# Performance work log

Hardware: AMD Instinct MI355X
Metric: run time of the kernel (lower is better)

## Reference

```python
import jax, jax.numpy as jnp
import numpy as np
import math

N_HEAD = 16
N_KV_HEAD = 4
N_EMBD = 2048
HEAD_DIM = N_EMBD // N_HEAD  # 128
SCALE = 1.0 / math.sqrt(HEAD_DIM)
B, T = 2, 2048


def setup_inputs() -> dict:
    key = jax.random.key(0)
    ks = jax.random.split(key, 5)
    s = 0.02
    x = jax.random.normal(ks[0], (B, T, N_EMBD), dtype=jnp.float32)
    wq = jax.random.normal(ks[1], (N_EMBD, N_EMBD), dtype=jnp.float32) * s
    wk = jax.random.normal(ks[2], (N_KV_HEAD * HEAD_DIM, N_EMBD), dtype=jnp.float32) * s
    wv = jax.random.normal(ks[3], (N_KV_HEAD * HEAD_DIM, N_EMBD), dtype=jnp.float32) * s
    wo = jax.random.normal(ks[4], (N_EMBD, N_EMBD), dtype=jnp.float32) * s
    return {"x": x, "wq": wq, "wk": wk, "wv": wv, "wo": wo}


def _forward(x, wq, wk, wv, wo):
    b, t, _ = x.shape
    # Linear layers: y = x @ W.T  (torch Linear weight is (out,in))
    q = (x @ wq.T).reshape(b, t, N_HEAD, HEAD_DIM).transpose(0, 2, 1, 3)      # (B,H,T,D)
    k = (x @ wk.T).reshape(b, t, N_KV_HEAD, HEAD_DIM).transpose(0, 2, 1, 3)  # (B,Hkv,T,D)
    v = (x @ wv.T).reshape(b, t, N_KV_HEAD, HEAD_DIM).transpose(0, 2, 1, 3)
    groups = N_HEAD // N_KV_HEAD
    k = jnp.repeat(k, groups, axis=1)  # repeat_interleave over head dim -> (B,H,T,D)
    v = jnp.repeat(v, groups, axis=1)
    # Causal mask: True above diagonal (masked-out positions)
    mask = jnp.triu(jnp.ones((t, t), dtype=bool), k=1)[None, None]  # (1,1,T,T)
    scores = jnp.einsum('bhqd,bhkd->bhqk', q, k) * SCALE
    scores = jnp.where(mask, -jnp.inf, scores)
    attn = jax.nn.softmax(scores, axis=-1)
    attn = jnp.where(mask, 0.0, attn)
    y = jnp.einsum('bhqk,bhkd->bhqd', attn, v)       # (B,H,T,D)
    y = y.transpose(0, 2, 1, 3).reshape(b, t, N_EMBD)
    return y @ wo.T


def reference(x, wq, wk, wv, wo):
    return _forward(x, wq, wk, wv, wo)
```

## Files before the change

### kernel.cpp

```cpp
#include <hip/hip_runtime.h>
#include <cstdint>
#include <cstddef>

typedef __bf16 bf16_t;
typedef __bf16 bf16x8 __attribute__((ext_vector_type(8)));
typedef __bf16 bf16x4 __attribute__((ext_vector_type(4)));
typedef float f32x4 __attribute__((ext_vector_type(4)));

#define GL2LDS16(gptr, lptr)                                                   \
  __builtin_amdgcn_global_load_lds(                                            \
      (__attribute__((address_space(1))) void*)(gptr),                         \
      (__attribute__((address_space(3))) void*)(lptr), 16, 0, 0)

__device__ __forceinline__ float fast_exp2(float x) {
  float r;
  asm volatile("v_exp_f32 %0, %1" : "=v"(r) : "v"(x));
  return r;
}

#define BATCH 2
#define T_SEQ 2048
#define NH 16
#define NKV 4
#define HD 128
#define EMB 2048
#define KVDIM (NKV * HD)
#define MROWS (BATCH * T_SEQ)

__global__ void cvt_all(const float4* __restrict__ x,  const float4* __restrict__ wq,
                        const float4* __restrict__ wk, const float4* __restrict__ wv,
                        const float4* __restrict__ wo,
                        bf16x4* __restrict__ xb,  bf16x4* __restrict__ wqb,
                        bf16x4* __restrict__ wkb, bf16x4* __restrict__ wvb,
                        bf16x4* __restrict__ wob) {
  const int blk = blockIdx.x;
  const float4* src;
  bf16x4* dst;
  int base;
  if (blk < 8192)       { src = x;  dst = xb;  base = blk; }
  else if (blk < 12288) { src = wq; dst = wqb; base = blk - 8192; }
  else if (blk < 13312) { src = wk; dst = wkb; base = blk - 12288; }
  else if (blk < 14336) { src = wv; dst = wvb; base = blk - 13312; }
  else                  { src = wo; dst = wob; base = blk - 14336; }
  const int i = base * 256 + threadIdx.x;
  const float4 v = src[i];
  dst[i] = bf16x4{(__bf16)v.x, (__bf16)v.y, (__bf16)v.z, (__bf16)v.w};
}

#define BK8 64
#define NT8 (EMB / BK8)

__global__ __launch_bounds__(512, 2)
void gemm_qkv8(const bf16_t* __restrict__ A,
               const bf16_t* __restrict__ Wq, const bf16_t* __restrict__ Wk,
               const bf16_t* __restrict__ Wv,
               bf16_t* __restrict__ Qb, bf16_t* __restrict__ Kb,
               bf16_t* __restrict__ Vt, float qalpha)
{
  __shared__ bf16_t lds[2][512 * 64];

  const int tid  = threadIdx.x;
  const int lane = tid & 63;
  const int wv   = tid >> 6;
  const int l15  = lane & 15;
  const int lq   = lane >> 4;

  const int bid0 = blockIdx.x;
  const int bid  = (bid0 & 7) * 24 + (bid0 >> 3);
  const int mt = bid / 12, nt = bid % 12;
  const int m0 = mt * 256;

  const bf16_t* Bmat; int ncol0, seg;
  if (nt < 8)       { Bmat = Wq; ncol0 = nt * 256;        seg = 0; }
  else if (nt < 10) { Bmat = Wk; ncol0 = (nt - 8) * 256;  seg = 1; }
  else              { Bmat = Wv; ncol0 = (nt - 10) * 256; seg = 2; }

  const int wm = (wv >> 2) * 128;
  const int wn = (wv & 3) * 64;

  f32x4 acc[8][4] = {};

  auto stage = [&](int dbuf, int tsrc, int h) {
    const int k0 = tsrc * BK8;
    const bf16_t* src = (h < 2) ? A : Bmat;
    const int rbase = (h < 2) ? (m0 + h * 128) : (ncol0 + (h - 2) * 128);
    bf16_t* dst = &lds[dbuf][h * 8192];
#pragma unroll
    for (int r = 0; r < 2; ++r) {
      const int c = r * 512 + tid;
      const int row = c >> 3, p = c & 7;
      const int sb = p ^ (row & 7);
      GL2LDS16(src + (size_t)(rbase + row) * EMB + k0 + sb * 8, dst + c * 8);
    }
  };

  auto ldA = [&](int buf, int half, bf16x8 (&dst)[4][2]) {
#pragma unroll
    for (int i = 0; i < 4; ++i) {
      const int row = wm + half * 64 + i * 16 + l15;
#pragma unroll
      for (int ks = 0; ks < 2; ++ks)
        dst[i][ks] = *(const bf16x8*)&lds[buf][row * 64 + (((ks * 4 + lq) ^ (row & 7)) * 8)];
    }
  };
  auto ldB = [&](int buf, int half, bf16x8 (&dst)[2][2]) {
#pragma unroll
    for (int j = 0; j < 2; ++j) {
      const int row = 256 + wn + half * 32 + j * 16 + l15;
#pragma unroll
      for (int ks = 0; ks < 2; ++ks)
        dst[j][ks] = *(const bf16x8*)&lds[buf][row * 64 + (((ks * 4 + lq) ^ (row & 7)) * 8)];
    }
  };
  auto mm = [&](bf16x8 (&Af)[4][2], bf16x8 (&Bf)[2][2], int ai, int bj) {
    __builtin_amdgcn_s_setprio(1);
#pragma unroll
    for (int ks = 0; ks < 2; ++ks)
#pragma unroll
      for (int i = 0; i < 4; ++i)
#pragma unroll
        for (int j = 0; j < 2; ++j)
          acc[ai + i][bj + j] = __builtin_amdgcn_mfma_f32_16x16x32_bf16(
              Af[i][ks], Bf[j][ks], acc[ai + i][bj + j], 0, 0, 0);
    __builtin_amdgcn_s_setprio(0);
  };

  stage(0, 0, 0); stage(0, 0, 1); stage(0, 0, 2); stage(0, 0, 3);
  stage(1, 1, 2); stage(1, 1, 0); stage(1, 1, 3);
  asm volatile("s_waitcnt vmcnt(6)" ::: "memory");
  __builtin_amdgcn_s_barrier();

  bf16x8 al[4][2], ah[4][2], bX[2][2], bY[2][2];
  ldA(0, 0, al);
  ldB(0, 0, bX);

  auto body = [&](int cur, int t, bf16x8 (&b01)[2][2], bf16x8 (&b23)[2][2]) {
    const int nxt = cur ^ 1;
    const int tn1 = (t + 1 < NT8) ? t + 1 : NT8 - 1;
    const int tn2 = (t + 2 < NT8) ? t + 2 : NT8 - 1;

    stage(nxt, tn1, 1);
    ldB(cur, 1, b23);
    mm(al, b01, 0, 0);
    __builtin_amdgcn_s_barrier();

    ldA(cur, 1, ah);
    mm(al, b23, 0, 2);
    __builtin_amdgcn_s_barrier();

    stage(cur, tn2, 2);
    mm(ah, b23, 4, 2);
    __builtin_amdgcn_s_barrier();

    asm volatile("s_waitcnt vmcnt(2)" ::: "memory");
    stage(cur, tn2, 0);
    stage(cur, tn2, 3);
    ldA(nxt, 0, al);
    ldB(nxt, 0, b23);
    mm(ah, b01, 4, 0);
    __builtin_amdgcn_s_barrier();
  };

#pragma unroll 1
  for (int tt = 0; tt < NT8; tt += 2) {
    body(0, tt,     bX, bY);
    body(1, tt + 1, bY, bX);
  }
  asm volatile("s_waitcnt vmcnt(0)" ::: "memory");

  if (seg == 0) {
#pragma unroll
    for (int i = 0; i < 8; ++i) {
      const int rbase = m0 + wm + i * 16 + lq * 4;
#pragma unroll
      for (int j = 0; j < 4; ++j) {
        const int col = ncol0 + wn + j * 16 + l15;
#pragma unroll
        for (int r = 0; r < 4; ++r)
          Qb[(size_t)(rbase + r) * EMB + col] = (bf16_t)(acc[i][j][r] * qalpha);
      }
    }
  } else if (seg == 1) {
#pragma unroll
    for (int i = 0; i < 8; ++i) {
      const int rbase = m0 + wm + i * 16 + lq * 4;
#pragma unroll
      for (int j = 0; j < 4; ++j) {
        const int col = ncol0 + wn + j * 16 + l15;
#pragma unroll
        for (int r = 0; r < 4; ++r)
          Kb[(size_t)(rbase + r) * KVDIM + col] = (bf16_t)acc[i][j][r];
      }
    }
  } else {
    const int bb = m0 >> 11;
    const int mloc0 = (m0 & 2047) + wm + lq * 4;
#pragma unroll
    for (int i = 0; i < 8; ++i) {
      const int mloc = mloc0 + i * 16;
#pragma unroll
      for (int j = 0; j < 4; ++j) {
        const int d = ncol0 + wn + j * 16 + l15;
        *(bf16x4*)(Vt + (size_t)(bb * KVDIM + d) * T_SEQ + mloc) =
            bf16x4{(__bf16)acc[i][j][0], (__bf16)acc[i][j][1],
                   (__bf16)acc[i][j][2], (__bf16)acc[i][j][3]};
      }
    }
  }
}

__global__ __launch_bounds__(256, 2)
void gemm_out(const bf16_t* __restrict__ A, const bf16_t* __restrict__ Bm,
              float* __restrict__ C, int M, int N, int K)
{
  __shared__ bf16_t As[128 * 64];
  __shared__ bf16_t Bs[128 * 64];

  const int tid  = threadIdx.x;
  const int lane = tid & 63;
  const int wv   = tid >> 6;
  const int m0 = blockIdx.y * 128;
  const int n0 = blockIdx.x * 128;
  const int wm = (wv >> 1) * 64;
  const int wn = (wv & 1) * 64;
  const int l15 = lane & 15;
  const int lq  = lane >> 4;

  f32x4 acc[4][4] = {};
  const int srow = tid >> 3;
  const int scol = (tid & 7) * 8;

  for (int k0 = 0; k0 < K; k0 += 64) {
#pragma unroll
    for (int r = 0; r < 4; ++r) {
      const int row = r * 32 + srow;
      GL2LDS16(A + (size_t)(m0 + row) * K + k0 + scol, As + row * 64 + scol);
    }
#pragma unroll
    for (int r = 0; r < 4; ++r) {
      const int row = r * 32 + srow;
      GL2LDS16(Bm + (size_t)(n0 + row) * K + k0 + scol, Bs + row * 64 + scol);
    }
    __syncthreads();

#pragma unroll
    for (int ks = 0; ks < 2; ++ks) {
      const int kc = ks * 32 + lq * 8;
      bf16x8 af[4], bf[4];
#pragma unroll
      for (int i = 0; i < 4; ++i)
        af[i] = *(const bf16x8*)(As + (wm + i * 16 + l15) * 64 + kc);
#pragma unroll
      for (int j = 0; j < 4; ++j)
        bf[j] = *(const bf16x8*)(Bs + (wn + j * 16 + l15) * 64 + kc);
#pragma unroll
      for (int i = 0; i < 4; ++i)
#pragma unroll
        for (int j = 0; j < 4; ++j)
          acc[i][j] = __builtin_amdgcn_mfma_f32_16x16x32_bf16(af[i], bf[j], acc[i][j], 0, 0, 0);
    }
    __syncthreads();
  }

#pragma unroll
  for (int i = 0; i < 4; ++i) {
    const int rbase = m0 + wm + i * 16 + lq * 4;
#pragma unroll
    for (int j = 0; j < 4; ++j) {
      const int col = n0 + wn + j * 16 + l15;
#pragma unroll
      for (int r = 0; r < 4; ++r)
        C[(size_t)(rbase + r) * N + col] = acc[i][j][r];
    }
  }
}

#define PSTR 72

__global__ __launch_bounds__(256, 2)
void attn_fwd(const bf16_t* __restrict__ Q, const bf16_t* __restrict__ Kg,
              const bf16_t* __restrict__ Vt, bf16_t* __restrict__ Y)
{
  __shared__ bf16_t Ks[2][64 * 128];
  __shared__ bf16_t Vs[2][128 * 64];
  __shared__ bf16_t Ps[4][16 * PSTR];

  const int tid  = threadIdx.x;
  const int lane = tid & 63;
  const int wv   = tid >> 6;
  const int l15  = lane & 15;
  const int lq   = lane >> 4;
  const int h  = blockIdx.y;
  const int b  = blockIdx.z;
  const int hkv = h >> 2;
  bf16_t* Psw = Ps[wv];

  auto stage = [&](int kt, int bufsel) {
    const int base_t = b * T_SEQ + kt * 64;
#pragma unroll
    for (int r = 0; r < 4; ++r) {
      const int c = r * 256 + tid;
      const int row = c >> 4, p = c & 15;
      const int sb = p ^ (row & 7);
      GL2LDS16(Kg + (size_t)(base_t + row) * KVDIM + hkv * HD + sb * 8,
               &Ks[bufsel][c * 8]);
    }
#pragma unroll
    for (int r = 0; r < 4; ++r) {
      const int c = r * 256 + tid;
      const int row = c >> 3, p = c & 7;
      const int sb = p ^ (row & 7);
      GL2LDS16(Vt + (size_t)(b * KVDIM + hkv * HD + row) * T_SEQ + kt * 64 + sb * 8,
               &Vs[bufsel][c * 8]);
    }
  };

#pragma unroll 1
  for (int ph = 0; ph < 2; ++ph) {
    const int qt = ph ? blockIdx.x : (31 - blockIdx.x);
    const int q0 = qt * 64;
    const int nkt = qt + 1;
    const int qabs = q0 + wv * 16 + l15;

    bf16x8 qf[4];
    {
      const bf16_t* qp = Q + ((size_t)(b * T_SEQ + qabs) * NH + h) * HD + lq * 8;
#pragma unroll
      for (int ds = 0; ds < 4; ++ds)
        qf[ds] = *(const bf16x8*)(qp + ds * 32);
    }

    float l_part = 0.f;
    f32x4 o[8];
#pragma unroll
    for (int nb = 0; nb < 8; ++nb) o[nb] = f32x4{0.f, 0.f, 0.f, 0.f};

    __syncthreads();
    stage(0, 0);

    for (int kt = 0; kt < nkt; ++kt) {
      const int cur = kt & 1;
      __syncthreads();
      if (kt + 1 < nkt) stage(kt + 1, cur ^ 1);

      f32x4 s[4];
#pragma unroll
      for (int nb = 0; nb < 4; ++nb) {
        s[nb] = f32x4{0.f, 0.f, 0.f, 0.f};
        const int row = nb * 16 + l15;
        const int r7  = row & 7;
#pragma unroll
        for (int ds = 0; ds < 4; ++ds) {
          const bf16x8 kf = *(const bf16x8*)&Ks[cur][row * 128 + (((ds * 4 + lq) ^ r7) * 8)];
          s[nb] = __builtin_amdgcn_mfma_f32_16x16x32_bf16(kf, qf[ds], s[nb], 0, 0, 0);
        }
      }

      const bool dia = (kt == nkt - 1);
#pragma unroll
      for (int nb = 0; nb < 4; ++nb) {
        const int kvb = kt * 64 + nb * 16 + lq * 4;
        float p0, p1, p2, p3;
        if (dia) {
          p0 = (kvb + 0 <= qabs) ? fast_exp2(s[nb][0]) : 0.f;
          p1 = (kvb + 1 <= qabs) ? fast_exp2(s[nb][1]) : 0.f;
          p2 = (kvb + 2 <= qabs) ? fast_exp2(s[nb][2]) : 0.f;
          p3 = (kvb + 3 <= qabs) ? fast_exp2(s[nb][3]) : 0.f;
        } else {
          p0 = fast_exp2(s[nb][0]);
          p1 = fast_exp2(s[nb][1]);
          p2 = fast_exp2(s[nb][2]);
          p3 = fast_exp2(s[nb][3]);
        }
        l_part += (p0 + p1) + (p2 + p3);
        *(bf16x4*)(Psw + l15 * PSTR + nb * 16 + lq * 4) =
            bf16x4{(__bf16)p0, (__bf16)p1, (__bf16)p2, (__bf16)p3};
      }

      asm volatile("s_waitcnt lgkmcnt(0)" ::: "memory");

#pragma unroll
      for (int ks = 0; ks < 2; ++ks) {
        const bf16x8 pf = *(const bf16x8*)(Psw + l15 * PSTR + ks * 32 + lq * 8);
#pragma unroll
        for (int nb = 0; nb < 8; ++nb) {
          const int row = nb * 16 + l15;
          const bf16x8 vf = *(const bf16x8*)&Vs[cur][row * 64 + (((ks * 4 + lq) ^ (row & 7)) * 8)];
          o[nb] = __builtin_amdgcn_mfma_f32_16x16x32_bf16(vf, pf, o[nb], 0, 0, 0);
        }
      }
    }

    float lt = l_part;
    lt += __shfl_xor(lt, 16);
    lt += __shfl_xor(lt, 32);
    const float inv = 1.f / lt;
    bf16_t* yp = Y + ((size_t)(b * T_SEQ + qabs) * NH + h) * HD + lq * 4;
#pragma unroll
    for (int nb = 0; nb < 8; ++nb) {
      *(bf16x4*)(yp + nb * 16) = bf16x4{(__bf16)(o[nb][0] * inv), (__bf16)(o[nb][1] * inv),
                                        (__bf16)(o[nb][2] * inv), (__bf16)(o[nb][3] * inv)};
    }
  }
}

extern "C" void kernel_launch(void* const* d_in, const int* in_sizes, int n_in,
                              void* d_out, int out_size, void* d_ws, size_t ws_size,
                              hipStream_t stream) {
  const float* x  = (const float*)d_in[0];
  const float* wq = (const float*)d_in[1];
  const float* wk = (const float*)d_in[2];
  const float* wv = (const float*)d_in[3];
  const float* wo = (const float*)d_in[4];
  float* out = (float*)d_out;

  const size_t n_x  = (size_t)MROWS * EMB;
  const size_t n_wq = (size_t)EMB * EMB;
  const size_t n_wk = (size_t)KVDIM * EMB;

  bf16_t* xb  = (bf16_t*)d_ws;
  bf16_t* wqb = xb  + n_x;
  bf16_t* wkb = wqb + n_wq;
  bf16_t* wvb = wkb + n_wk;
  bf16_t* wob = wvb + n_wk;
  bf16_t* Qb  = wob + n_wq;
  bf16_t* Kb  = Qb + (size_t)MROWS * EMB;
  bf16_t* Vtb = Kb + (size_t)MROWS * KVDIM;
  bf16_t* Yb  = Vtb + (size_t)MROWS * KVDIM;

  dim3 blk(256);

  cvt_all<<<dim3(18432), blk, 0, stream>>>(
      (const float4*)x, (const float4*)wq, (const float4*)wk, (const float4*)wv, (const float4*)wo,
      (bf16x4*)xb, (bf16x4*)wqb, (bf16x4*)wkb, (bf16x4*)wvb, (bf16x4*)wob);

  const float qalpha = 0.08838834764831845f * 1.4426950408889634f;
  gemm_qkv8<<<dim3(192), dim3(512), 0, stream>>>(xb, wqb, wkb, wvb,
                                                 Qb, Kb, Vtb, qalpha);

  attn_fwd<<<dim3(16, NH, BATCH), blk, 0, stream>>>(Qb, Kb, Vtb, Yb);

  gemm_out<<<dim3(EMB / 128, MROWS / 128), blk, 0, stream>>>(Yb, wob, out, MROWS, EMB, EMB);
}
```

Measured before the change: 316.9 us.

## Restructure QKV GEMM pipeline to stage whole tiles per iteration with simpler double buffering

Replaces the fine-grained per-quarter staging schedule, which interleaved four partial global-to-LDS loads across the four MFMA phases, with a single-iteration loop. Each iteration now stages the entire K-tile two steps ahead into the current buffer after that buffer has been consumed, and waits with vmcnt(0) mid-iteration. The intent is a simpler schedule with less loop-carried register swapping and separate LDS arrays. The cost is that loads are issued in one burst and fully drained each iteration, which may expose more memory latency than the staggered scheme.

```diff
diff --git a/kernel.cpp b/kernel.cpp
--- a/kernel.cpp
+++ b/kernel.cpp
@@ -50,6 +50,38 @@
 #define BK8 64
 #define NT8 (EMB / BK8)
 
+#define LDA(dst, buf, half)                                                    \
+  _Pragma("unroll")                                                            \
+  for (int i_ = 0; i_ < 4; ++i_) {                                             \
+    const int row_ = wm + (half) * 64 + i_ * 16 + l15;                         \
+    _Pragma("unroll")                                                          \
+    for (int ks_ = 0; ks_ < 2; ++ks_)                                          \
+      dst[i_][ks_] = *(const bf16x8*)&(buf)[row_ * 64 +                        \
+                                            (((ks_ * 4 + lq) ^ (row_ & 7)) * 8)]; \
+  }
+
+#define LDB(dst, buf, qoff)                                                    \
+  _Pragma("unroll")                                                            \
+  for (int j_ = 0; j_ < 2; ++j_) {                                             \
+    const int row_ = 256 + wn + (qoff) + j_ * 16 + l15;                        \
+    _Pragma("unroll")                                                          \
+    for (int ks_ = 0; ks_ < 2; ++ks_)                                          \
+      dst[j_][ks_] = *(const bf16x8*)&(buf)[row_ * 64 +                        \
+                                            (((ks_ * 4 + lq) ^ (row_ & 7)) * 8)]; \
+  }
+
+#define MM(Af, Bf, ai, bj)                                                     \
+  __builtin_amdgcn_s_setprio(1);                                               \
+  _Pragma("unroll")                                                            \
+  for (int ks_ = 0; ks_ < 2; ++ks_)                                            \
+    _Pragma("unroll")                                                          \
+    for (int i_ = 0; i_ < 4; ++i_)                                             \
+      _Pragma("unroll")                                                        \
+      for (int j_ = 0; j_ < 2; ++j_)                                           \
+        acc[(ai) + i_][(bj) + j_] = __builtin_amdgcn_mfma_f32_16x16x32_bf16(   \
+            Af[i_][ks_], Bf[j_][ks_], acc[(ai) + i_][(bj) + j_], 0, 0, 0);     \
+  __builtin_amdgcn_s_setprio(0);
+
 __global__ __launch_bounds__(512, 2)
 void gemm_qkv8(const bf16_t* __restrict__ A,
                const bf16_t* __restrict__ Wq, const bf16_t* __restrict__ Wk,
@@ -57,7 +89,8 @@
                bf16_t* __restrict__ Qb, bf16_t* __restrict__ Kb,
                bf16_t* __restrict__ Vt, float qalpha)
 {
-  __shared__ bf16_t lds[2][512 * 64];
+  __shared__ bf16_t lds0[512 * 64];
+  __shared__ bf16_t lds1[512 * 64];
 
   const int tid  = threadIdx.x;
   const int lane = tid & 63;
@@ -80,91 +113,55 @@
 
   f32x4 acc[8][4] = {};
 
-  auto stage = [&](int dbuf, int tsrc, int h) {
+  auto stageAll = [&](bf16_t* dstbuf, int tsrc) {
     const int k0 = tsrc * BK8;
-    const bf16_t* src = (h < 2) ? A : Bmat;
-    const int rbase = (h < 2) ? (m0 + h * 128) : (ncol0 + (h - 2) * 128);
-    bf16_t* dst = &lds[dbuf][h * 8192];
-#pragma unroll
-    for (int r = 0; r < 2; ++r) {
-      const int c = r * 512 + tid;
-      const int row = c >> 3, p = c & 7;
-      const int sb = p ^ (row & 7);
-      GL2LDS16(src + (size_t)(rbase + row) * EMB + k0 + sb * 8, dst + c * 8);
+#pragma unroll
+    for (int h = 0; h < 4; ++h) {
+      const bf16_t* src = (h < 2) ? A : Bmat;
+      const int rbase = (h < 2) ? (m0 + h * 128) : (ncol0 + (h - 2) * 128);
+      bf16_t* dst = dstbuf + h * 8192;
+#pragma unroll
+      for (int r = 0; r < 2; ++r) {
+        const int c = r * 512 + tid;
+        const int row = c >> 3, p = c & 7;
+        const int sb = p ^ (row & 7);
+        GL2LDS16(src + (size_t)(rbase + row) * EMB + k0 + sb * 8, dst + c * 8);
+      }
     }
   };
 
-  auto ldA = [&](int buf, int half, bf16x8 (&dst)[4][2]) {
-#pragma unroll
-    for (int i = 0; i < 4; ++i) {
-      const int row = wm + half * 64 + i * 16 + l15;
-#pragma unroll
-      for (int ks = 0; ks < 2; ++ks)
-        dst[i][ks] = *(const bf16x8*)&lds[buf][row * 64 + (((ks * 4 + lq) ^ (row & 7)) * 8)];
-    }
-  };
-  auto ldB = [&](int buf, int half, bf16x8 (&dst)[2][2]) {
-#pragma unroll
-    for (int j = 0; j < 2; ++j) {
-      const int row = 256 + wn + half * 32 + j * 16 + l15;
-#pragma unroll
-      for (int ks = 0; ks < 2; ++ks)
-        dst[j][ks] = *(const bf16x8*)&lds[buf][row * 64 + (((ks * 4 + lq) ^ (row & 7)) * 8)];
-    }
-  };
-  auto mm = [&](bf16x8 (&Af)[4][2], bf16x8 (&Bf)[2][2], int ai, int bj) {
-    __builtin_amdgcn_s_setprio(1);
-#pragma unroll
-    for (int ks = 0; ks < 2; ++ks)
-#pragma unroll
-      for (int i = 0; i < 4; ++i)
-#pragma unroll
-        for (int j = 0; j < 2; ++j)
-          acc[ai + i][bj + j] = __builtin_amdgcn_mfma_f32_16x16x32_bf16(
-              Af[i][ks], Bf[j][ks], acc[ai + i][bj + j], 0, 0, 0);
-    __builtin_amdgcn_s_setprio(0);
-  };
-
-  stage(0, 0, 0); stage(0, 0, 1); stage(0, 0, 2); stage(0, 0, 3);
-  stage(1, 1, 2); stage(1, 1, 0); stage(1, 1, 3);
-  asm volatile("s_waitcnt vmcnt(6)" ::: "memory");
+  stageAll(lds0, 0);
+  stageAll(lds1, 1);
+  asm volatile("s_waitcnt vmcnt(8)" ::: "memory");
   __builtin_amdgcn_s_barrier();
 
-  bf16x8 al[4][2], ah[4][2], bX[2][2], bY[2][2];
-  ldA(0, 0, al);
-  ldB(0, 0, bX);
-
-  auto body = [&](int cur, int t, bf16x8 (&b01)[2][2], bf16x8 (&b23)[2][2]) {
-    const int nxt = cur ^ 1;
-    const int tn1 = (t + 1 < NT8) ? t + 1 : NT8 - 1;
+  bf16x8 a03[4][2], a47[4][2], b01[2][2], b23[2][2];
+  LDA(a03, lds0, 0);
+  LDB(b01, lds0, 0);
+
+#pragma unroll 1
+  for (int t = 0; t < NT8; ++t) {
+    bf16_t* curb = (t & 1) ? lds1 : lds0;
+    bf16_t* nxtb = (t & 1) ? lds0 : lds1;
     const int tn2 = (t + 2 < NT8) ? t + 2 : NT8 - 1;
 
-    stage(nxt, tn1, 1);
-    ldB(cur, 1, b23);
-    mm(al, b01, 0, 0);
+    LDB(b23, curb, 32);
+    MM(a03, b01, 0, 0);
     __builtin_amdgcn_s_barrier();
 
-    ldA(cur, 1, ah);
-    mm(al, b23, 0, 2);
+    LDA(a47, curb, 1);
+    MM(a03, b23, 0, 2);
+    asm volatile("s_waitcnt vmcnt(0)" ::: "memory");
     __builtin_amdgcn_s_barrier();
 
-    stage(cur, tn2, 2);
-    mm(ah, b23, 4, 2);
+    LDA(a03, nxtb, 0);
+    MM(a47, b01, 4, 0);
     __builtin_amdgcn_s_barrier();
 
-    asm volatile("s_waitcnt vmcnt(2)" ::: "memory");
-    stage(cur, tn2, 0);
-    stage(cur, tn2, 3);
-    ldA(nxt, 0, al);
-    ldB(nxt, 0, b23);
-    mm(ah, b01, 4, 0);
+    stageAll(curb, tn2);
+    LDB(b01, nxtb, 0);
+    MM(a47, b23, 4, 2);
     __builtin_amdgcn_s_barrier();
-  };
-
-#pragma unroll 1
-  for (int tt = 0; tt < NT8; tt += 2) {
-    body(0, tt,     bX, bY);
-    body(1, tt + 1, bY, bX);
   }
   asm volatile("s_waitcnt vmcnt(0)" ::: "memory");
 
```

New measurement: 282.4 us. 10.9% less time.
